# Kernel optimization log

Hardware: AMD Instinct MI355X
Metric: run time of the kernel (lower is better)

Reference implementation:

```python
import jax, jax.numpy as jnp
import numpy as np

NUM_HEADS = 16
TOP_K = 2

def setup_inputs() -> dict:
    key = jax.random.key(0)
    ks = jax.random.split(key, 5)
    B, D, E = 8192, 2048, 8
    x = jax.random.normal(ks[0], (B, D), dtype=jnp.float32)
    W_qkv = jax.random.normal(ks[1], (E, D, 3 * D), dtype=jnp.float32) * 0.02  # (in,out) per expert
    W_gate = jax.random.normal(ks[2], (D, E), dtype=jnp.float32) * 0.02
    b_gate = jnp.zeros((E,), dtype=jnp.float32)
    W_proj = jax.random.normal(ks[3], (D, D), dtype=jnp.float32) * 0.02
    b_proj = jnp.zeros((D,), dtype=jnp.float32)
    return {"x": x, "W_qkv": W_qkv, "W_gate": W_gate, "b_gate": b_gate,
            "W_proj": W_proj, "b_proj": b_proj}


def reference(x, W_qkv, W_gate, b_gate, W_proj, b_proj):
    B, D = x.shape
    E = W_qkv.shape[0]
    H = NUM_HEADS
    hd = D // H
    scale = float(hd) ** -0.5

    # gating + top-k (sparse gate weights, zeros for non-selected experts)
    gate_scores = jax.nn.softmax(x @ W_gate + b_gate, axis=-1)        # (B, E)
    topk_vals, topk_idx = jax.lax.top_k(gate_scores, TOP_K)           # (B, K)
    gw = jnp.zeros_like(gate_scores).at[jnp.arange(B)[:, None], topk_idx].add(topk_vals)

    # gate-weighted combine of expert QKV projections (linear => combine after GEMM)
    qkv = jnp.zeros((B, 3 * D), dtype=x.dtype)
    for e in range(E):  # fixed small expert count; each iter is one big GEMM
        qkv = qkv + gw[:, e:e + 1] * (x @ W_qkv[e])
    qkv = qkv.reshape(B, 3, H, hd)

    # NOTE: the torch source writes `q = k = v = torch.zeros(...)` then uses
    # in-place `+=`, so q, k, v ALIAS one tensor: all equal gate*(q_i+k_i+v_i).
    # We replicate that exact math faithfully.
    s = qkv.sum(axis=1)                                               # (B, H, hd)

    attn = jax.nn.softmax(jnp.einsum('bhd,bgd->bhg', s, s) * scale, axis=-1)  # (B, H, H)
    out = jnp.einsum('bhg,bgd->bhd', attn, s)                         # (B, H, hd)
    out = out.transpose(0, 2, 1).reshape(B, D)                        # matches .transpose(1,2).reshape
    return out @ W_proj + b_proj
```

## Files before the change

kernel.cpp:

```cpp
#include <hip/hip_runtime.h>

#define B_ROWS 8192
#define DDIM 2048
#define NEXP 8
#define NASSIGN (B_ROWS * 2)
#define MAX_TILES 80

typedef unsigned short u16;
typedef short bf16x8 __attribute__((ext_vector_type(8)));
typedef float f32x4 __attribute__((ext_vector_type(4)));

#define M_CNT 0
#define M_FILL 8
#define M_SEG 16
#define M_TE 32
#define M_TB 112
#define M_TR 192

__device__ __forceinline__ u16 f2b(float f) {
  union { float f; unsigned u; } c; c.f = f;
  return (u16)((c.u + 0x7fffu + ((c.u >> 16) & 1u)) >> 16);
}
__device__ __forceinline__ float b2f(u16 h) {
  union { unsigned u; float f; } c; c.u = ((unsigned)h) << 16;
  return c.f;
}
__device__ __forceinline__ void async16(u16* lds, const u16* g) {
  __builtin_amdgcn_global_load_lds(
      (const __attribute__((address_space(1))) unsigned int*)g,
      (__attribute__((address_space(3))) unsigned int*)lds, 16, 0, 0);
}

__global__ void init_meta_kernel(int* meta) {
  int t = threadIdx.x;
  if (t < 16) meta[t] = 0;
}

template <int NSUM>
__global__ __launch_bounds__(256) void prep_transpose(
    const float* __restrict__ Win, u16* __restrict__ Wout, int ldin) {
  __shared__ u16 tl[64][72];
  int bx = blockIdx.x;
  int nt = bx & 31, kt = (bx >> 5) & 31, e = bx >> 10;
  int t = threadIdx.x;
  const size_t in_base = (size_t)e * DDIM * (size_t)ldin;
  int k0 = kt * 64, n0 = nt * 64;
#pragma unroll
  for (int i = 0; i < 4; ++i) {
    int idx = i * 256 + t;
    int kl = idx >> 4, f4 = idx & 15;
    const float* p = Win + in_base + (size_t)(k0 + kl) * ldin + n0 + f4 * 4;
    float4 v = *(const float4*)p;
    if (NSUM == 3) {
      float4 v1 = *(const float4*)(p + 2048);
      float4 v2 = *(const float4*)(p + 4096);
      v.x += v1.x + v2.x; v.y += v1.y + v2.y;
      v.z += v1.z + v2.z; v.w += v1.w + v2.w;
    }
    tl[f4 * 4 + 0][kl] = f2b(v.x);
    tl[f4 * 4 + 1][kl] = f2b(v.y);
    tl[f4 * 4 + 2][kl] = f2b(v.z);
    tl[f4 * 4 + 3][kl] = f2b(v.w);
  }
  __syncthreads();
  u16* out = Wout + (size_t)e * DDIM * DDIM;
#pragma unroll
  for (int i = 0; i < 2; ++i) {
    int idx = i * 256 + t;
    int nl = idx >> 3, kc = idx & 7;
    const u16* r = &tl[nl][kc * 8];
    uint4 pk;
    pk.x = (unsigned)r[0] | ((unsigned)r[1] << 16);
    pk.y = (unsigned)r[2] | ((unsigned)r[3] << 16);
    pk.z = (unsigned)r[4] | ((unsigned)r[5] << 16);
    pk.w = (unsigned)r[6] | ((unsigned)r[7] << 16);
    *(uint4*)(out + (size_t)(n0 + nl) * DDIM + k0 + kc * 8) = pk;
  }
}

__global__ __launch_bounds__(256) void gate_kernel(
    const float* __restrict__ x, const float* __restrict__ Wg,
    const float* __restrict__ bg, u16* __restrict__ xb,
    int* __restrict__ e01, float* __restrict__ w01, int* __restrict__ meta) {
  int b = blockIdx.x, t = threadIdx.x;
  const float* xr = x + (size_t)b * DDIM;
  float4 v0 = ((const float4*)xr)[2 * t];
  float4 v1 = ((const float4*)xr)[2 * t + 1];
  float xv[8] = {v0.x, v0.y, v0.z, v0.w, v1.x, v1.y, v1.z, v1.w};
  uint4 pk;
  pk.x = (unsigned)f2b(xv[0]) | ((unsigned)f2b(xv[1]) << 16);
  pk.y = (unsigned)f2b(xv[2]) | ((unsigned)f2b(xv[3]) << 16);
  pk.z = (unsigned)f2b(xv[4]) | ((unsigned)f2b(xv[5]) << 16);
  pk.w = (unsigned)f2b(xv[6]) | ((unsigned)f2b(xv[7]) << 16);
  *(uint4*)(xb + (size_t)b * DDIM + t * 8) = pk;

  double acc[8] = {0, 0, 0, 0, 0, 0, 0, 0};
#pragma unroll
  for (int j = 0; j < 8; ++j) {
    const float4* wr = (const float4*)(Wg + (size_t)(t * 8 + j) * 8);
    float4 wa = wr[0], wb = wr[1];
    double xd = (double)xv[j];
    acc[0] += xd * wa.x; acc[1] += xd * wa.y;
    acc[2] += xd * wa.z; acc[3] += xd * wa.w;
    acc[4] += xd * wb.x; acc[5] += xd * wb.y;
    acc[6] += xd * wb.z; acc[7] += xd * wb.w;
  }
#pragma unroll
  for (int e = 0; e < 8; ++e)
    for (int m2 = 32; m2; m2 >>= 1) acc[e] += __shfl_xor(acc[e], m2);
  __shared__ double red[4][8];
  if ((t & 63) == 0)
    for (int e = 0; e < 8; ++e) red[t >> 6][e] = acc[e];
  __syncthreads();
  if (t == 0) {
    double l[8];
    for (int e = 0; e < 8; ++e)
      l[e] = red[0][e] + red[1][e] + red[2][e] + red[3][e] + (double)bg[e];
    double mx = l[0];
    for (int e = 1; e < 8; ++e) mx = l[e] > mx ? l[e] : mx;
    double p[8], s = 0;
    for (int e = 0; e < 8; ++e) { p[e] = exp(l[e] - mx); s += p[e]; }
    int i1 = 0;
    for (int e = 1; e < 8; ++e) if (p[e] > p[i1]) i1 = e;
    int i2 = (i1 == 0) ? 1 : 0;
    for (int e = 0; e < 8; ++e)
      if (e != i1 && p[e] > p[i2]) i2 = e;
    e01[2 * b] = i1; e01[2 * b + 1] = i2;
    w01[2 * b] = (float)(p[i1] / s);
    w01[2 * b + 1] = (float)(p[i2] / s);
    atomicAdd(&meta[M_CNT + i1], 1);
    atomicAdd(&meta[M_CNT + i2], 1);
  }
}

__global__ void scan_kernel(int* meta) {
  if (threadIdx.x != 0) return;
  int total = 0;
  for (int e = 0; e < 8; ++e) { meta[M_SEG + e] = total; total += meta[M_CNT + e]; }
  int tt = 0;
  for (int e = 0; e < 8; ++e) {
    int cnt = meta[M_CNT + e];
    int ntl = (cnt + 255) >> 8;
    for (int i = 0; i < ntl; ++i) {
      meta[M_TE + tt] = e;
      meta[M_TB + tt] = meta[M_SEG + e] + i * 256;
      meta[M_TR + tt] = cnt - i * 256;
      ++tt;
    }
  }
  for (; tt < MAX_TILES; ++tt) { meta[M_TE + tt] = 0; meta[M_TB + tt] = 0; meta[M_TR + tt] = 0; }
}

__global__ __launch_bounds__(256) void build_kernel(
    const int* __restrict__ e01, const float* __restrict__ w01,
    int* __restrict__ meta, int* __restrict__ rows, float* __restrict__ wt,
    int* __restrict__ rowpos) {
  int b = blockIdx.x * 256 + threadIdx.x;
  if (b >= B_ROWS) return;
#pragma unroll
  for (int s = 0; s < 2; ++s) {
    int e = e01[2 * b + s];
    float w = w01[2 * b + s];
    int p = meta[M_SEG + e] + atomicAdd(&meta[M_FILL + e], 1);
    rows[p] = b;
    wt[p] = w;
    rowpos[2 * b + s] = p;
  }
}

#define BAR()                           \
  do {                                  \
    __builtin_amdgcn_sched_barrier(0);  \
    __builtin_amdgcn_s_barrier();       \
    __builtin_amdgcn_sched_barrier(0);  \
  } while (0)
#define VMCNT2() asm volatile("s_waitcnt vmcnt(2)" ::: "memory")
#define VMCNT0() asm volatile("s_waitcnt vmcnt(0)" ::: "memory")
#define LGKM0()                                       \
  do {                                                \
    asm volatile("s_waitcnt lgkmcnt(0)" ::: "memory"); \
    __builtin_amdgcn_sched_barrier(0);                \
  } while (0)

#define STAGE_A(L, T, BB) async16(&lds[BB][0][(L)*4096 + t * 8], srcA[L] + (size_t)(T)*64)
#define STAGE_B(L, T, BB) async16(&lds[BB][1][(L)*4096 + t * 8], srcB[L] + (size_t)(T)*64)

#define READ_A(QM)                                                   \
  do {                                                               \
    _Pragma("unroll") for (int i_ = 0; i_ < 4; ++i_) {               \
      int rb_ = baseA + ((QM)*64 + i_ * 16) * 128;                   \
      af[i_][0] = *(const bf16x8*)(pA + rb_ + ck0);                  \
      af[i_][1] = *(const bf16x8*)(pA + rb_ + ck1);                  \
    }                                                                \
  } while (0)
#define READ_B(H)                                                    \
  do {                                                               \
    _Pragma("unroll") for (int j_ = 0; j_ < 2; ++j_) {               \
      int rb_ = baseB + (((H)*2 + j_) * 16) * 128;                   \
      bfr[(H)*2 + j_][0] = *(const bf16x8*)(pB + rb_ + ck0);         \
      bfr[(H)*2 + j_][1] = *(const bf16x8*)(pB + rb_ + ck1);         \
    }                                                                \
  } while (0)
#define MFMA16(QM, QN)                                                         \
  do {                                                                         \
    _Pragma("unroll") for (int i_ = 0; i_ < 4; ++i_) {                         \
      _Pragma("unroll") for (int j_ = 0; j_ < 2; ++j_) {                       \
        acc[(QM)*4 + i_][(QN)*2 + j_] = __builtin_amdgcn_mfma_f32_16x16x32_bf16( \
            af[i_][0], bfr[(QN)*2 + j_][0], acc[(QM)*4 + i_][(QN)*2 + j_], 0, 0, 0); \
        acc[(QM)*4 + i_][(QN)*2 + j_] = __builtin_amdgcn_mfma_f32_16x16x32_bf16( \
            af[i_][1], bfr[(QN)*2 + j_][1], acc[(QM)*4 + i_][(QN)*2 + j_], 0, 0, 0); \
      }                                                                        \
    }                                                                          \
  } while (0)

template <int MODE>
__global__ __launch_bounds__(512, 2) void gemm256_kernel(
    const u16* __restrict__ A, const u16* __restrict__ BT,
    const int* __restrict__ meta, const int* __restrict__ rows,
    const float* __restrict__ wt, const float* __restrict__ bias,
    u16* __restrict__ Yc, float* __restrict__ Out) {
  __shared__ __align__(16) u16 lds[2][2][16384];

  int e = 0, base = 0, rem = 256, m0 = 0;
  if (MODE == 0) {
    rem = meta[M_TR + blockIdx.y];
    if (rem <= 0) return;
    if (rem > 256) rem = 256;
    e = meta[M_TE + blockIdx.y];
    base = meta[M_TB + blockIdx.y];
  } else {
    m0 = blockIdx.y * 256;
  }
  const int n0 = blockIdx.x * 256;
  const int t = threadIdx.x;
  const int lane = t & 63;
  const int wid = t >> 6;
  const int wr = wid >> 2, wc = wid & 3;
  const int l15 = lane & 15;
  const int kg = lane >> 4;
  const int sw = lane & 7;

  const u16* srcA[4];
  const u16* srcB[4];
#pragma unroll
  for (int L = 0; L < 4; ++L) {
    int row = L * 64 + (t >> 3);
    int cl = (t & 7) ^ (row & 7);
    int grow;
    if (MODE == 0) {
      int rl = row < rem ? row : 0;
      grow = rows[base + rl];
    } else {
      grow = m0 + row;
    }
    srcA[L] = A + (size_t)grow * DDIM + cl * 8;
    srcB[L] = BT + ((size_t)e * DDIM + n0 + row) * DDIM + cl * 8;
  }

  f32x4 acc[8][4];
#pragma unroll
  for (int i = 0; i < 8; ++i)
#pragma unroll
    for (int j = 0; j < 4; ++j) {
      f32x4 z = {0.f, 0.f, 0.f, 0.f};
      acc[i][j] = z;
    }

  const int baseA = (wr * 128 + l15) * 128;
  const int baseB = (wc * 64 + l15) * 128;
  const int ck0 = ((0 * 4 + kg) ^ sw) << 4;
  const int ck1 = ((1 * 4 + kg) ^ sw) << 4;

  bf16x8 af[4][2];
  bf16x8 bfr[4][2];

  STAGE_A(0, 0, 0); STAGE_A(1, 0, 0); STAGE_A(2, 0, 0); STAGE_A(3, 0, 0);
  STAGE_B(0, 0, 0); STAGE_B(1, 0, 0); STAGE_B(2, 0, 0); STAGE_B(3, 0, 0);
  STAGE_A(0, 1, 1); STAGE_A(1, 1, 1);
  VMCNT2();
  BAR();

  const int NT = DDIM / 64;
  for (int T = 0; T < NT; ++T) {
    const int cb = T & 1, nb = cb ^ 1;
    const char* pA = (const char*)&lds[cb][0][0];
    const char* pB = (const char*)&lds[cb][1][0];
    READ_A(0);
    READ_B(0);
    if (T + 1 < NT) { STAGE_A(2, T + 1, nb); STAGE_A(3, T + 1, nb); }
    BAR();
    LGKM0();
    __builtin_amdgcn_s_setprio(1);
    MFMA16(0, 0);
    __builtin_amdgcn_s_setprio(0);
    BAR();
    READ_B(1);
    if (T + 1 < NT) { STAGE_B(0, T + 1, nb); STAGE_B(1, T + 1, nb); }
    BAR();
    LGKM0();
    __builtin_amdgcn_s_setprio(1);
    MFMA16(0, 1);
    __builtin_amdgcn_s_setprio(0);
    BAR();
    READ_A(1);
    if (T + 1 < NT) { STAGE_B(2, T + 1, nb); STAGE_B(3, T + 1, nb); }
    BAR();
    LGKM0();
    __builtin_amdgcn_s_setprio(1);
    MFMA16(1, 0);
    __builtin_amdgcn_s_setprio(0);
    BAR();
    if (T + 2 < NT) {
      STAGE_A(0, T + 2, cb); STAGE_A(1, T + 2, cb);
      VMCNT2();
    } else {
      VMCNT0();
    }
    BAR();
    __builtin_amdgcn_s_setprio(1);
    MFMA16(1, 1);
    __builtin_amdgcn_s_setprio(0);
    BAR();
  }

  if (MODE == 1) {
    float bv[4];
#pragma unroll
    for (int fn = 0; fn < 4; ++fn) bv[fn] = bias[n0 + wc * 64 + fn * 16 + l15];
#pragma unroll
    for (int qm = 0; qm < 2; ++qm)
#pragma unroll
      for (int i = 0; i < 4; ++i)
#pragma unroll
        for (int r = 0; r < 4; ++r) {
          int rl = wr * 128 + qm * 64 + i * 16 + kg * 4 + r;
          float* orow = Out + (size_t)(m0 + rl) * DDIM + n0 + wc * 64 + l15;
#pragma unroll
          for (int fn = 0; fn < 4; ++fn)
            orow[fn * 16] = acc[qm * 4 + i][fn][r] + bv[fn];
        }
  } else {
#pragma unroll
    for (int qm = 0; qm < 2; ++qm)
#pragma unroll
      for (int i = 0; i < 4; ++i)
#pragma unroll
        for (int r = 0; r < 4; ++r) {
          int rl = wr * 128 + qm * 64 + i * 16 + kg * 4 + r;
          if (rl < rem) {
            int pos = base + rl;
            float w = wt[pos];
            u16* yrow = Yc + (size_t)pos * DDIM + n0 + wc * 64 + l15;
#pragma unroll
            for (int fn = 0; fn < 4; ++fn)
              yrow[fn * 16] = f2b(w * acc[qm * 4 + i][fn][r]);
          }
        }
  }
}

__global__ __launch_bounds__(256) void combine_attn_kernel(
    const u16* __restrict__ Yc, const int* __restrict__ rowpos,
    u16* __restrict__ ab) {
  __shared__ __align__(16) float sm[16][132];
  __shared__ float at[16][17];
  __shared__ __align__(16) float osm[16][132];
  int b = blockIdx.x, t = threadIdx.x;
  int p0 = rowpos[2 * b], p1 = rowpos[2 * b + 1];
  uint4 ya = *(const uint4*)(Yc + (size_t)p0 * DDIM + t * 8);
  uint4 yb = *(const uint4*)(Yc + (size_t)p1 * DDIM + t * 8);
  const unsigned* au = (const unsigned*)&ya;
  const unsigned* bu = (const unsigned*)&yb;
  float v[8];
#pragma unroll
  for (int j = 0; j < 4; ++j) {
    v[2 * j] = b2f((u16)(au[j] & 0xffff)) + b2f((u16)(bu[j] & 0xffff));
    v[2 * j + 1] = b2f((u16)(au[j] >> 16)) + b2f((u16)(bu[j] >> 16));
  }
  {
    int row = t >> 4, col = (t & 15) * 8;
    float4 w0 = {v[0], v[1], v[2], v[3]};
    float4 w1 = {v[4], v[5], v[6], v[7]};
    *(float4*)&sm[row][col] = w0;
    *(float4*)&sm[row][col + 4] = w1;
  }
  __syncthreads();
  const int h = t >> 4, g = t & 15;
  {
    const float4* sh4 = (const float4*)&sm[h][0];
    const float4* sg4 = (const float4*)&sm[g][0];
    float4 a4 = {0.f, 0.f, 0.f, 0.f};
#pragma unroll
    for (int j = 0; j < 32; ++j) {
      float4 xa = sh4[j], xc = sg4[j];
      a4.x += xa.x * xc.x; a4.y += xa.y * xc.y;
      a4.z += xa.z * xc.z; a4.w += xa.w * xc.w;
    }
    float dot = (a4.x + a4.y) + (a4.z + a4.w);
    float lg = dot * 0.088388347648318447f;
    float mx = lg;
#pragma unroll
    for (int m2 = 8; m2; m2 >>= 1) mx = fmaxf(mx, __shfl_xor(mx, m2, 16));
    float ex = expf(lg - mx);
    float sum = ex;
#pragma unroll
    for (int m2 = 8; m2; m2 >>= 1) sum += __shfl_xor(sum, m2, 16);
    at[h][g] = ex / sum;
  }
  __syncthreads();
  {
    const int c = t & 15;
    float4 o0 = {0.f, 0.f, 0.f, 0.f};
    float4 o1 = {0.f, 0.f, 0.f, 0.f};
#pragma unroll
    for (int gg = 0; gg < 16; ++gg) {
      float w = at[h][gg];
      float4 s0 = *(const float4*)&sm[gg][c * 4];
      float4 s1 = *(const float4*)&sm[gg][64 + c * 4];
      o0.x += w * s0.x; o0.y += w * s0.y; o0.z += w * s0.z; o0.w += w * s0.w;
      o1.x += w * s1.x; o1.y += w * s1.y; o1.z += w * s1.z; o1.w += w * s1.w;
    }
    *(float4*)&osm[h][c * 4] = o0;
    *(float4*)&osm[h][64 + c * 4] = o1;
  }
  __syncthreads();
  uint4 pk;
  unsigned w2[4];
#pragma unroll
  for (int j = 0; j < 4; ++j) {
    int f0 = t * 8 + 2 * j, f1 = t * 8 + 2 * j + 1;
    w2[j] = (unsigned)f2b(osm[f0 & 15][f0 >> 4]) |
            ((unsigned)f2b(osm[f1 & 15][f1 >> 4]) << 16);
  }
  pk.x = w2[0]; pk.y = w2[1]; pk.z = w2[2]; pk.w = w2[3];
  *(uint4*)(ab + (size_t)b * DDIM + t * 8) = pk;
}

extern "C" void kernel_launch(void* const* d_in, const int* in_sizes, int n_in,
                              void* d_out, int out_size, void* d_ws, size_t ws_size,
                              hipStream_t stream) {
  const float* x = (const float*)d_in[0];
  const float* Wqkv = (const float*)d_in[1];
  const float* Wg = (const float*)d_in[2];
  const float* bg = (const float*)d_in[3];
  const float* Wp = (const float*)d_in[4];
  const float* bp = (const float*)d_in[5];
  float* out = (float*)d_out;

  char* ws = (char*)d_ws;
  size_t off = 0;
  auto alloc = [&](size_t bytes) {
    void* p = ws + off;
    off += (bytes + 255) & ~(size_t)255;
    return p;
  };
  u16* xb = (u16*)alloc((size_t)B_ROWS * DDIM * 2);
  u16* WsumT = (u16*)alloc((size_t)NEXP * DDIM * DDIM * 2);
  u16* WprojT = (u16*)alloc((size_t)DDIM * DDIM * 2);
  u16* Yc = (u16*)alloc((size_t)NASSIGN * DDIM * 2);
  u16* ab = (u16*)alloc((size_t)B_ROWS * DDIM * 2);
  int* e01 = (int*)alloc((size_t)NASSIGN * 4);
  float* w01 = (float*)alloc((size_t)NASSIGN * 4);
  int* rows = (int*)alloc((size_t)NASSIGN * 4);
  float* wt = (float*)alloc((size_t)NASSIGN * 4);
  int* rowpos = (int*)alloc((size_t)NASSIGN * 4);
  int* meta = (int*)alloc(4096);

  init_meta_kernel<<<dim3(1), dim3(64), 0, stream>>>(meta);
  prep_transpose<3><<<dim3(NEXP * 32 * 32), dim3(256), 0, stream>>>(Wqkv, WsumT, 3 * DDIM);
  prep_transpose<1><<<dim3(32 * 32), dim3(256), 0, stream>>>(Wp, WprojT, DDIM);
  gate_kernel<<<dim3(B_ROWS), dim3(256), 0, stream>>>(x, Wg, bg, xb, e01, w01, meta);
  scan_kernel<<<dim3(1), dim3(64), 0, stream>>>(meta);
  build_kernel<<<dim3(32), dim3(256), 0, stream>>>(e01, w01, meta, rows, wt, rowpos);
  gemm256_kernel<0><<<dim3(8, MAX_TILES), dim3(512), 0, stream>>>(
      xb, WsumT, meta, rows, wt, nullptr, Yc, nullptr);
  combine_attn_kernel<<<dim3(B_ROWS), dim3(256), 0, stream>>>(Yc, rowpos, ab);
  gemm256_kernel<1><<<dim3(8, 32), dim3(512), 0, stream>>>(
      ab, WprojT, meta, rows, wt, bp, nullptr, out);
  (void)in_sizes; (void)n_in; (void)out_size; (void)ws_size;
}
```

Measured before the change: 699.0 us.

## Make GEMMs persistent with XCD-aware atomic tile scheduling

Both GEMM launches become persistent grids of 256 blocks that take work items from per-XCD atomic counters. The M-tiles are split into 8 groups, one per XCD, ordered so that paired M-tiles share B columns, with work stealing across groups once a group runs dry. This is meant to stop launching empty padded tiles, improve L2 reuse inside each XCD, and balance the uneven per-expert tile counts. In exchange it adds atomic and barrier overhead per tile and depends on the hardware XCC_ID register read.

```diff
diff --git a/kernel.cpp b/kernel.cpp
--- a/kernel.cpp
+++ b/kernel.cpp
@@ -13,9 +13,12 @@
 #define M_CNT 0
 #define M_FILL 8
 #define M_SEG 16
-#define M_TE 32
-#define M_TB 112
-#define M_TR 192
+#define M_CTRA 24
+#define M_CTRB 32
+#define M_NT 40
+#define M_TE 48
+#define M_TB 128
+#define M_TR 208
 
 __device__ __forceinline__ u16 f2b(float f) {
   union { float f; unsigned u; } c; c.f = f;
@@ -33,7 +36,7 @@
 
 __global__ void init_meta_kernel(int* meta) {
   int t = threadIdx.x;
-  if (t < 16) meta[t] = 0;
+  if (t < 48) meta[t] = 0;
 }
 
 template <int NSUM>
@@ -148,6 +151,7 @@
       ++tt;
     }
   }
+  meta[M_NT] = tt;
   for (; tt < MAX_TILES; ++tt) { meta[M_TE + tt] = 0; meta[M_TB + tt] = 0; meta[M_TR + tt] = 0; }
 }
 
@@ -216,22 +220,12 @@
 template <int MODE>
 __global__ __launch_bounds__(512, 2) void gemm256_kernel(
     const u16* __restrict__ A, const u16* __restrict__ BT,
-    const int* __restrict__ meta, const int* __restrict__ rows,
+    int* __restrict__ meta, const int* __restrict__ rows,
     const float* __restrict__ wt, const float* __restrict__ bias,
     u16* __restrict__ Yc, float* __restrict__ Out) {
   __shared__ __align__(16) u16 lds[2][2][16384];
-
-  int e = 0, base = 0, rem = 256, m0 = 0;
-  if (MODE == 0) {
-    rem = meta[M_TR + blockIdx.y];
-    if (rem <= 0) return;
-    if (rem > 256) rem = 256;
-    e = meta[M_TE + blockIdx.y];
-    base = meta[M_TB + blockIdx.y];
-  } else {
-    m0 = blockIdx.y * 256;
-  }
-  const int n0 = blockIdx.x * 256;
+  __shared__ int s_w;
+
   const int t = threadIdx.x;
   const int lane = t & 63;
   const int wid = t >> 6;
@@ -239,123 +233,172 @@
   const int l15 = lane & 15;
   const int kg = lane >> 4;
   const int sw = lane & 7;
-
-  const u16* srcA[4];
-  const u16* srcB[4];
-#pragma unroll
-  for (int L = 0; L < 4; ++L) {
-    int row = L * 64 + (t >> 3);
-    int cl = (t & 7) ^ (row & 7);
-    int grow;
-    if (MODE == 0) {
-      int rl = row < rem ? row : 0;
-      grow = rows[base + rl];
-    } else {
-      grow = m0 + row;
-    }
-    srcA[L] = A + (size_t)grow * DDIM + cl * 8;
-    srcB[L] = BT + ((size_t)e * DDIM + n0 + row) * DDIM + cl * 8;
-  }
-
-  f32x4 acc[8][4];
-#pragma unroll
-  for (int i = 0; i < 8; ++i)
-#pragma unroll
-    for (int j = 0; j < 4; ++j) {
-      f32x4 z = {0.f, 0.f, 0.f, 0.f};
-      acc[i][j] = z;
-    }
-
   const int baseA = (wr * 128 + l15) * 128;
   const int baseB = (wc * 64 + l15) * 128;
   const int ck0 = ((0 * 4 + kg) ^ sw) << 4;
   const int ck1 = ((1 * 4 + kg) ^ sw) << 4;
 
-  bf16x8 af[4][2];
-  bf16x8 bfr[4][2];
-
-  STAGE_A(0, 0, 0); STAGE_A(1, 0, 0); STAGE_A(2, 0, 0); STAGE_A(3, 0, 0);
-  STAGE_B(0, 0, 0); STAGE_B(1, 0, 0); STAGE_B(2, 0, 0); STAGE_B(3, 0, 0);
-  STAGE_A(0, 1, 1); STAGE_A(1, 1, 1);
-  VMCNT2();
-  BAR();
-
-  const int NT = DDIM / 64;
-  for (int T = 0; T < NT; ++T) {
-    const int cb = T & 1, nb = cb ^ 1;
-    const char* pA = (const char*)&lds[cb][0][0];
-    const char* pB = (const char*)&lds[cb][1][0];
-    READ_A(0);
-    READ_B(0);
-    if (T + 1 < NT) { STAGE_A(2, T + 1, nb); STAGE_A(3, T + 1, nb); }
+  const int nt = (MODE == 0) ? meta[M_NT] : 32;
+  const int ctrbase = (MODE == 0) ? M_CTRA : M_CTRB;
+
+  int xcd;
+  asm volatile("s_getreg_b32 %0, hwreg(20, 0, 4)" : "=s"(xcd));
+  xcd &= 7;
+
+  int q = 0;
+
+  for (;;) {
+    if (t == 0) {
+      int pk = -1;
+      while (q < 8) {
+        int qq = (xcd + q) & 7;
+        int tlo_ = (qq * nt) >> 3;
+        int cnt_ = (((qq + 1) * nt) >> 3) - tlo_;
+        int w = atomicAdd(&meta[ctrbase + qq], 1);
+        if (w < cnt_ * 8) { pk = (qq << 16) | w; break; }
+        ++q;
+      }
+      s_w = pk;
+    }
+    __syncthreads();
+    const int pk = s_w;
+    if (pk < 0) return;
+    const int qq = pk >> 16, w = pk & 0xffff;
+    const int tlo = (qq * nt) >> 3;
+    const int cnt = (((qq + 1) * nt) >> 3) - tlo;
+    const int fp = cnt >> 1;
+    int mt, n0i;
+    if (w < fp * 16) {
+      mt = tlo + ((w >> 4) << 1) + (w & 1);
+      n0i = (w >> 1) & 7;
+    } else {
+      mt = tlo + cnt - 1;
+      n0i = w - fp * 16;
+    }
+    const int n0 = n0i << 8;
+
+    int e = 0, base = 0, rem = 256, m0 = 0;
+    if (MODE == 0) {
+      rem = meta[M_TR + mt];
+      if (rem > 256) rem = 256;
+      e = meta[M_TE + mt];
+      base = meta[M_TB + mt];
+    } else {
+      m0 = mt << 8;
+    }
+
+    const u16* srcA[4];
+    const u16* srcB[4];
+#pragma unroll
+    for (int L = 0; L < 4; ++L) {
+      int row = L * 64 + (t >> 3);
+      int cl = (t & 7) ^ (row & 7);
+      int grow;
+      if (MODE == 0) {
+        int rl = row < rem ? row : 0;
+        grow = rows[base + rl];
+      } else {
+        grow = m0 + row;
+      }
+      srcA[L] = A + (size_t)grow * DDIM + cl * 8;
+      srcB[L] = BT + ((size_t)e * DDIM + n0 + row) * DDIM + cl * 8;
+    }
+
+    f32x4 acc[8][4];
+#pragma unroll
+    for (int i = 0; i < 8; ++i)
+#pragma unroll
+      for (int j = 0; j < 4; ++j) {
+        f32x4 z = {0.f, 0.f, 0.f, 0.f};
+        acc[i][j] = z;
+      }
+
+    bf16x8 af[4][2];
+    bf16x8 bfr[4][2];
+
+    STAGE_A(0, 0, 0); STAGE_A(1, 0, 0); STAGE_A(2, 0, 0); STAGE_A(3, 0, 0);
+    STAGE_B(0, 0, 0); STAGE_B(1, 0, 0); STAGE_B(2, 0, 0); STAGE_B(3, 0, 0);
+    STAGE_A(0, 1, 1); STAGE_A(1, 1, 1);
+    VMCNT2();
     BAR();
-    LGKM0();
-    __builtin_amdgcn_s_setprio(1);
-    MFMA16(0, 0);
-    __builtin_amdgcn_s_setprio(0);
-    BAR();
-    READ_B(1);
-    if (T + 1 < NT) { STAGE_B(0, T + 1, nb); STAGE_B(1, T + 1, nb); }
-    BAR();
-    LGKM0();
-    __builtin_amdgcn_s_setprio(1);
-    MFMA16(0, 1);
-    __builtin_amdgcn_s_setprio(0);
-    BAR();
-    READ_A(1);
-    if (T + 1 < NT) { STAGE_B(2, T + 1, nb); STAGE_B(3, T + 1, nb); }
-    BAR();
-    LGKM0();
-    __builtin_amdgcn_s_setprio(1);
-    MFMA16(1, 0);
-    __builtin_amdgcn_s_setprio(0);
-    BAR();
-    if (T + 2 < NT) {
-      STAGE_A(0, T + 2, cb); STAGE_A(1, T + 2, cb);
-      VMCNT2();
+
+    const int NT = DDIM / 64;
+    for (int T = 0; T < NT; ++T) {
+      const int cb = T & 1, nb = cb ^ 1;
+      const char* pA = (const char*)&lds[cb][0][0];
+      const char* pB = (const char*)&lds[cb][1][0];
+      READ_A(0);
+      READ_B(0);
+      if (T + 1 < NT) { STAGE_A(2, T + 1, nb); STAGE_A(3, T + 1, nb); }
+      BAR();
+      LGKM0();
+      __builtin_amdgcn_s_setprio(1);
+      MFMA16(0, 0);
+      __builtin_amdgcn_s_setprio(0);
+      BAR();
+      READ_B(1);
+      if (T + 1 < NT) { STAGE_B(0, T + 1, nb); STAGE_B(1, T + 1, nb); }
+      BAR();
+      LGKM0();
+      __builtin_amdgcn_s_setprio(1);
+      MFMA16(0, 1);
+      __builtin_amdgcn_s_setprio(0);
+      BAR();
+      READ_A(1);
+      if (T + 1 < NT) { STAGE_B(2, T + 1, nb); STAGE_B(3, T + 1, nb); }
+      BAR();
+      LGKM0();
+      __builtin_amdgcn_s_setprio(1);
+      MFMA16(1, 0);
+      __builtin_amdgcn_s_setprio(0);
+      BAR();
+      if (T + 2 < NT) {
+        STAGE_A(0, T + 2, cb); STAGE_A(1, T + 2, cb);
+        VMCNT2();
+      } else {
+        VMCNT0();
+      }
+      BAR();
+      __builtin_amdgcn_s_setprio(1);
+      MFMA16(1, 1);
+      __builtin_amdgcn_s_setprio(0);
+      BAR();
+    }
+
+    if (MODE == 1) {
+      float bv[4];
+#pragma unroll
+      for (int fn = 0; fn < 4; ++fn) bv[fn] = bias[n0 + wc * 64 + fn * 16 + l15];
+#pragma unroll
+      for (int qm = 0; qm < 2; ++qm)
+#pragma unroll
+        for (int i = 0; i < 4; ++i)
+#pragma unroll
+          for (int r = 0; r < 4; ++r) {
+            int rl = wr * 128 + qm * 64 + i * 16 + kg * 4 + r;
+            float* orow = Out + (size_t)(m0 + rl) * DDIM + n0 + wc * 64 + l15;
+#pragma unroll
+            for (int fn = 0; fn < 4; ++fn)
+              orow[fn * 16] = acc[qm * 4 + i][fn][r] + bv[fn];
+          }
     } else {
-      VMCNT0();
-    }
-    BAR();
-    __builtin_amdgcn_s_setprio(1);
-    MFMA16(1, 1);
-    __builtin_amdgcn_s_setprio(0);
-    BAR();
-  }
-
-  if (MODE == 1) {
-    float bv[4];
-#pragma unroll
-    for (int fn = 0; fn < 4; ++fn) bv[fn] = bias[n0 + wc * 64 + fn * 16 + l15];
-#pragma unroll
-    for (int qm = 0; qm < 2; ++qm)
-#pragma unroll
-      for (int i = 0; i < 4; ++i)
-#pragma unroll
-        for (int r = 0; r < 4; ++r) {
-          int rl = wr * 128 + qm * 64 + i * 16 + kg * 4 + r;
-          float* orow = Out + (size_t)(m0 + rl) * DDIM + n0 + wc * 64 + l15;
-#pragma unroll
-          for (int fn = 0; fn < 4; ++fn)
-            orow[fn * 16] = acc[qm * 4 + i][fn][r] + bv[fn];
-        }
-  } else {
-#pragma unroll
-    for (int qm = 0; qm < 2; ++qm)
-#pragma unroll
-      for (int i = 0; i < 4; ++i)
-#pragma unroll
-        for (int r = 0; r < 4; ++r) {
-          int rl = wr * 128 + qm * 64 + i * 16 + kg * 4 + r;
-          if (rl < rem) {
-            int pos = base + rl;
-            float w = wt[pos];
-            u16* yrow = Yc + (size_t)pos * DDIM + n0 + wc * 64 + l15;
-#pragma unroll
-            for (int fn = 0; fn < 4; ++fn)
-              yrow[fn * 16] = f2b(w * acc[qm * 4 + i][fn][r]);
+#pragma unroll
+      for (int qm = 0; qm < 2; ++qm)
+#pragma unroll
+        for (int i = 0; i < 4; ++i)
+#pragma unroll
+          for (int r = 0; r < 4; ++r) {
+            int rl = wr * 128 + qm * 64 + i * 16 + kg * 4 + r;
+            if (rl < rem) {
+              int pos = base + rl;
+              float w2 = wt[pos];
+              u16* yrow = Yc + (size_t)pos * DDIM + n0 + wc * 64 + l15;
+#pragma unroll
+              for (int fn = 0; fn < 4; ++fn)
+                yrow[fn * 16] = f2b(w2 * acc[qm * 4 + i][fn][r]);
+            }
           }
-        }
+    }
   }
 }
 
@@ -472,10 +515,10 @@
   gate_kernel<<<dim3(B_ROWS), dim3(256), 0, stream>>>(x, Wg, bg, xb, e01, w01, meta);
   scan_kernel<<<dim3(1), dim3(64), 0, stream>>>(meta);
   build_kernel<<<dim3(32), dim3(256), 0, stream>>>(e01, w01, meta, rows, wt, rowpos);
-  gemm256_kernel<0><<<dim3(8, MAX_TILES), dim3(512), 0, stream>>>(
+  gemm256_kernel<0><<<dim3(256), dim3(512), 0, stream>>>(
       xb, WsumT, meta, rows, wt, nullptr, Yc, nullptr);
   combine_attn_kernel<<<dim3(B_ROWS), dim3(256), 0, stream>>>(Yc, rowpos, ab);
-  gemm256_kernel<1><<<dim3(8, 32), dim3(512), 0, stream>>>(
+  gemm256_kernel<1><<<dim3(256), dim3(512), 0, stream>>>(
       ab, WprojT, meta, rows, wt, bp, nullptr, out);
   (void)in_sizes; (void)n_in; (void)out_size; (void)ws_size;
 }
```

Result: slower. 734.0 us (+5.0%).
